# Kernel tuning notes

Measured on AMD Instinct MI355X. Metric: run time of the kernel, lower is better.

The kernel has to match this reference:

```python
import jax, jax.numpy as jnp
import numpy as np

EPS = 1e-5
DT_RANK = 64
N_STATE = 16


def _rmsnorm(x, w):
    var = jnp.mean(x * x, axis=-1, keepdims=True)
    return x * jax.lax.rsqrt(var + EPS) * w


def _softplus(x, beta=1.0, threshold=20.0):
    return jnp.where(beta * x > threshold, x, (1.0 / beta) * jnp.logaddexp(0.0, beta * x))


def _silu(x):
    return x * jax.nn.sigmoid(x)


def setup_inputs() -> dict:
    key = jax.random.key(0)
    ks = jax.random.split(key, 8)
    B, L, H = 2, 1024, 2048  # hidden_size = expand * d_model = 2048
    s = 0.02
    A = jnp.tile(jnp.arange(1.0, N_STATE + 1.0)[None, :], (H, 1))  # (H, 16)
    return {
        "x": jax.random.normal(ks[0], (B, L, H), jnp.float32),
        "norm_w": jnp.ones((H,), jnp.float32),
        "in_proj_w": jax.random.normal(ks[1], (2 * H, H), jnp.float32) * s,
        "conv_w": jax.random.normal(ks[2], (4, H, H), jnp.float32) * s,  # (K, Cin, Cout) LIO
        "conv_b": jnp.zeros((H,), jnp.float32),
        "x_proj_w": jax.random.normal(ks[3], (DT_RANK + 2 * N_STATE, H), jnp.float32) * s,
        "dt_proj_w": jax.random.normal(ks[4], (H, DT_RANK), jnp.float32) * s,
        "dt_proj_b": jnp.zeros((H,), jnp.float32),
        "A_log": jnp.log(A),
        "D": jnp.ones((H,), jnp.float32),
        "out_proj_w": jax.random.normal(ks[5], (H, H), jnp.float32) * s,
    }


def _scan_combine(left, right):
    aL, xL = left
    aR, xR = right
    return aR * aL, aR * xL + xR


def reference(x, norm_w, in_proj_w, conv_w, conv_b, x_proj_w, dt_proj_w, dt_proj_b, A_log, D, out_proj_w):
    B, L, H = x.shape
    h = _rmsnorm(x, norm_w)
    xz = h @ in_proj_w.T                      # (B, L, 2H)
    xc, z = jnp.split(xz, 2, axis=-1)         # each (B, L, H)
    # causal conv1d: mlx pads k-1 both sides then takes first L -> left pad only
    xc = jax.lax.conv_general_dilated(
        xc, conv_w, window_strides=(1,), padding=[(3, 0)],
        dimension_numbers=("NLC", "LIO", "NLC")) + conv_b
    xc = _silu(xc)
    # SSM
    A = -jnp.exp(A_log)                       # (H, N)
    dBC = xc @ x_proj_w.T                     # (B, L, dt_rank + 2N)
    delta = dBC[..., :DT_RANK]
    Bm = dBC[..., DT_RANK:DT_RANK + N_STATE]  # (B, L, N)
    Cm = dBC[..., DT_RANK + N_STATE:]         # (B, L, N)
    delta = _softplus(delta @ dt_proj_w.T + dt_proj_b)  # (B, L, H)
    deltaA = jnp.exp(delta[..., None] * A)              # (B, L, H, N)
    BX = (delta * xc)[..., None] * Bm[:, :, None, :]    # (B, L, H, N)
    _, hs = jax.lax.associative_scan(_scan_combine, (deltaA, BX), axis=1)
    y = jnp.einsum("blhn,bln->blh", hs, Cm) + D * xc
    out = (y * _silu(z)) @ out_proj_w.T
    return x + out
```

## Files before the change

kernel.cpp:

```cpp
#include <hip/hip_runtime.h>
#include <math.h>

typedef unsigned short u16;
typedef __bf16 bf16x8 __attribute__((ext_vector_type(8)));
typedef float f32x4 __attribute__((ext_vector_type(4)));
typedef unsigned short u16x8 __attribute__((ext_vector_type(8)));
typedef unsigned short u16x4 __attribute__((ext_vector_type(4)));

#define H 2048
#define LSEQ 1024
#define LP (LSEQ+3)
#define CL 32
#define NCH 32

__device__ __forceinline__ float bf2f(u16 u) {
    union { float f; unsigned int i; } x; x.i = ((unsigned int)u) << 16; return x.f;
}
__device__ __forceinline__ u16 f2bf(float f) {
    union { float f; unsigned int i; } x; x.f = f;
    unsigned int r = x.i + 0x7fffu + ((x.i >> 16) & 1u);
    return (u16)(r >> 16);
}

__device__ __forceinline__ void gload_lds16(const void* g, void* l) {
    __builtin_amdgcn_global_load_lds((const __attribute__((address_space(1))) void*)g,
                                     (__attribute__((address_space(3))) void*)l,
                                     16, 0, 0);
}

enum { EPI_XZ = 0, EPI_DELTA = 1, EPI_STORE = 5, EPI_P2 = 6 };

template<int EPI, bool APAD>
__launch_bounds__(512, 2)
__global__ void gemmA(const u16* __restrict__ A, const u16* __restrict__ B,
                      int lda, int ldb, long aZoff, long bZoff, int iters,
                      void* __restrict__ out0, void* __restrict__ out1,
                      void* __restrict__ out2, const float* __restrict__ aux) {
    __shared__ u16 As[5][128 * 32];
    __shared__ u16 Bs[5][256 * 32];
    const int flat = blockIdx.x + gridDim.x * (blockIdx.y + gridDim.y * blockIdx.z);
    const int xr = flat & 7;
    const int jj = flat >> 3;
    const int panel = xr + 8 * (jj >> 4);
    const int mI = jj & 15;
    const int m0 = mI * 128;
    const int yI = panel % gridDim.y;
    const int z  = panel / gridDim.y;
    const int n0 = yI * 256;
    const int tid = threadIdx.x;
    const int lane = tid & 63;
    const int w = tid >> 6;
    const int wr = w >> 2;
    const int wc = w & 3;

    long abase;
    if (APAD) {
        int b = m0 >> 10, l0 = m0 & 1023;
        abase = (long)(b * LP + l0) * lda;
    } else {
        abase = (long)m0 * lda;
    }
    const u16* Ag = A + abase + (long)z * aZoff;
    const u16* Bg = B + (long)n0 * ldb + (long)z * bZoff;

    const int sw8 = ((((lane & 15) >> 1) & 3) ^ (lane >> 4)) * 8;

    f32x4 acc[4][4];
#pragma unroll
    for (int i = 0; i < 4; i++)
#pragma unroll
        for (int j = 0; j < 4; j++) acc[i][j] = (f32x4){0.f, 0.f, 0.f, 0.f};

#define STG(s, bi)                                                                \
    {                                                                             \
        const int k0_ = (s) * 32;                                                 \
        {                                                                         \
            const int rA_ = tid >> 2;                                             \
            const int sgA_ = ((tid & 3) ^ ((rA_ >> 1) & 3)) * 8;                  \
            gload_lds16(Ag + (long)rA_ * lda + k0_ + sgA_, &As[bi][tid * 8]);     \
        }                                                                         \
        _Pragma("unroll")                                                         \
        for (int l_ = 0; l_ < 2; l_++) {                                          \
            const int idx_ = l_ * 512 + tid;                                      \
            const int rB_ = idx_ >> 2;                                            \
            const int sgB_ = ((idx_ & 3) ^ ((rB_ >> 1) & 3)) * 8;                 \
            gload_lds16(Bg + (long)rB_ * ldb + k0_ + sgB_, &Bs[bi][idx_ * 8]);    \
        }                                                                         \
    }

    STG(0, 0);
    if (iters > 1) STG(1, 1);
    if (iters > 2) STG(2, 2);
    if (iters > 3) STG(3, 3);
    {
        const int pre = iters < 4 ? iters : 4;
        if      (pre == 4) asm volatile("s_waitcnt vmcnt(9)" ::: "memory");
        else if (pre == 3) asm volatile("s_waitcnt vmcnt(6)" ::: "memory");
        else if (pre == 2) asm volatile("s_waitcnt vmcnt(3)" ::: "memory");
        else               asm volatile("s_waitcnt vmcnt(0)" ::: "memory");
    }
    __builtin_amdgcn_s_barrier();
    __builtin_amdgcn_sched_barrier(0);

    int cur = 0;
    for (int t = 0; t < iters; ++t) {
        const int sb = cur ? cur - 1 : 4;
        if (t + 4 < iters) STG(t + 4, sb);

        bf16x8 af[4], bfr[4];
#pragma unroll
        for (int i = 0; i < 4; i++) {
            const int row = wr * 64 + i * 16 + (lane & 15);
            af[i] = *(const bf16x8*)&As[cur][row * 32 + sw8];
        }
#pragma unroll
        for (int j = 0; j < 4; j++) {
            const int row = wc * 64 + j * 16 + (lane & 15);
            bfr[j] = *(const bf16x8*)&Bs[cur][row * 32 + sw8];
        }
        __builtin_amdgcn_s_setprio(1);
#pragma unroll
        for (int i = 0; i < 4; i++)
#pragma unroll
            for (int j = 0; j < 4; j++)
                acc[i][j] = __builtin_amdgcn_mfma_f32_16x16x32_bf16(af[i], bfr[j], acc[i][j], 0, 0, 0);
        __builtin_amdgcn_s_setprio(0);

        if (t < iters - 1) {
            const int lastst = (t + 4 < iters - 1) ? t + 4 : iters - 1;
            const int ahead = lastst - (t + 1);
            if      (ahead >= 3) asm volatile("s_waitcnt vmcnt(9)" ::: "memory");
            else if (ahead == 2) asm volatile("s_waitcnt vmcnt(6)" ::: "memory");
            else if (ahead == 1) asm volatile("s_waitcnt vmcnt(3)" ::: "memory");
            else                 asm volatile("s_waitcnt vmcnt(0)" ::: "memory");
            __builtin_amdgcn_s_barrier();
            __builtin_amdgcn_sched_barrier(0);
        }
        cur = (cur == 4) ? 0 : cur + 1;
    }
#undef STG

#pragma unroll
    for (int i = 0; i < 4; i++) {
#pragma unroll
        for (int j = 0; j < 4; j++) {
#pragma unroll
            for (int r = 0; r < 4; r++) {
                const int m = m0 + wr * 64 + i * 16 + ((lane >> 4) << 2) + r;
                const int n = n0 + wc * 64 + j * 16 + (lane & 15);
                float v = acc[i][j][r];
                if constexpr (EPI == EPI_XZ) {
                    const int b = m >> 10, l = m & 1023;
                    if (n < H) ((u16*)out0)[((long)(b * LP + l + 3)) * H + n] = f2bf(v);
                    else       ((u16*)out1)[(long)m * H + (n - H)] = f2bf(v);
                } else {
                    if (z == 0) {
                        ((float*)out0)[(long)m * H + n] = v;
                    } else {
                        float* p = (m < 1024) ? (float*)out1 : (float*)out2;
                        p[(long)(m & 1023) * H + n] = v;
                    }
                }
            }
        }
    }
}

template<int EPI, bool APAD>
__launch_bounds__(256)
__global__ void gemm_bt(const u16* __restrict__ A, const u16* __restrict__ B,
                        int K, long aZoff, long bZoff, int itersZ, int ldc,
                        void* __restrict__ out0, void* __restrict__ out1,
                        const float* __restrict__ bias) {
    __shared__ u16 As[128 * 32];
    __shared__ u16 Bs[128 * 32];
    const int m0 = blockIdx.x * 128;
    const int n0 = blockIdx.y * 128;
    const int z  = blockIdx.z;
    const int tid = threadIdx.x;
    const int lane = tid & 63;
    const int w = tid >> 6;
    const int wr = w >> 1, wc = w & 1;

    long abase = (long)m0 * K;
    const u16* Ag = A + abase + (long)z * aZoff;
    const u16* Bg = B + (long)n0 * K + (long)z * bZoff;

    const int sw8 = ((((lane & 15) >> 1) & 3) ^ (lane >> 4)) * 8;

    f32x4 acc[4][4];
#pragma unroll
    for (int i = 0; i < 4; i++)
#pragma unroll
        for (int j = 0; j < 4; j++) acc[i][j] = (f32x4){0.f, 0.f, 0.f, 0.f};

    for (int kt = 0; kt < itersZ; ++kt) {
        const int k0 = kt * 32;
        __syncthreads();
#pragma unroll
        for (int j = 0; j < 2; j++) {
            const int idx = j * 256 + tid;
            const int r = idx >> 2;
            const int segG = ((idx & 3) ^ ((r >> 1) & 3)) * 8;
            gload_lds16(Ag + (long)r * K + k0 + segG, &As[idx * 8]);
            gload_lds16(Bg + (long)r * K + k0 + segG, &Bs[idx * 8]);
        }
        __syncthreads();
        bf16x8 af[4], bfr[4];
#pragma unroll
        for (int i = 0; i < 4; i++) {
            const int row = wr * 64 + i * 16 + (lane & 15);
            af[i] = *(const bf16x8*)&As[row * 32 + sw8];
        }
#pragma unroll
        for (int j = 0; j < 4; j++) {
            const int row = wc * 64 + j * 16 + (lane & 15);
            bfr[j] = *(const bf16x8*)&Bs[row * 32 + sw8];
        }
#pragma unroll
        for (int i = 0; i < 4; i++)
#pragma unroll
            for (int j = 0; j < 4; j++)
                acc[i][j] = __builtin_amdgcn_mfma_f32_16x16x32_bf16(af[i], bfr[j], acc[i][j], 0, 0, 0);
    }

#pragma unroll
    for (int i = 0; i < 4; i++) {
#pragma unroll
        for (int j = 0; j < 4; j++) {
#pragma unroll
            for (int r = 0; r < 4; r++) {
                const int m = m0 + wr * 64 + i * 16 + ((lane >> 4) << 2) + r;
                const int n = n0 + wc * 64 + j * 16 + (lane & 15);
                float v = acc[i][j][r];
                if constexpr (EPI == EPI_DELTA) {
                    v += bias[n];
                    v = (v > 20.f) ? v : log1pf(expf(v));
                    ((float*)out0)[(long)m * H + n] = v;
                }
            }
        }
    }
}

template<int EPI, bool APAD>
__launch_bounds__(256)
__global__ void gemm128d(const u16* __restrict__ A, const u16* __restrict__ B,
                         int lda, int ldb, int iters,
                         long aZoff, long bZoff, long oZoff, int ldo,
                         void* __restrict__ out0, void* __restrict__ out1,
                         const float* __restrict__ aux) {
    __shared__ u16 As[6][128 * 32];
    __shared__ u16 Bs[6][128 * 32];
    const int m0 = blockIdx.y * 128;
    const int n0 = blockIdx.x * 128;
    const int z  = blockIdx.z;
    const int tid = threadIdx.x;
    const int lane = tid & 63;
    const int w = tid >> 6;
    const int wr = w >> 1, wc = w & 1;

    long abase = (long)m0 * lda;
    const u16* Ag = A + abase + (long)z * aZoff;
    const u16* Bg = B + (long)n0 * ldb + (long)z * bZoff;

    const int sw8 = ((((lane & 15) >> 1) & 3) ^ (lane >> 4)) * 8;

    f32x4 acc[4][4];
#pragma unroll
    for (int i = 0; i < 4; i++)
#pragma unroll
        for (int j = 0; j < 4; j++) acc[i][j] = (f32x4){0.f, 0.f, 0.f, 0.f};

#define STG(s, bi)                                                                \
    {                                                                             \
        const int k0_ = (s) * 32;                                                 \
        _Pragma("unroll")                                                         \
        for (int l_ = 0; l_ < 2; l_++) {                                          \
            const int idx_ = l_ * 256 + tid;                                      \
            const int r_ = idx_ >> 2;                                             \
            const int segG_ = ((idx_ & 3) ^ ((r_ >> 1) & 3)) * 8;                 \
            gload_lds16(Ag + (long)r_ * lda + k0_ + segG_, &As[bi][idx_ * 8]);    \
            gload_lds16(Bg + (long)r_ * ldb + k0_ + segG_, &Bs[bi][idx_ * 8]);    \
        }                                                                         \
    }

    STG(0, 0);
    if (iters > 1) STG(1, 1);
    if (iters > 2) STG(2, 2);
    if (iters > 3) STG(3, 3);
    if (iters > 4) STG(4, 4);
    {
        const int pre = iters < 5 ? iters : 5;
        if      (pre == 5) asm volatile("s_waitcnt vmcnt(16)" ::: "memory");
        else if (pre == 4) asm volatile("s_waitcnt vmcnt(12)" ::: "memory");
        else if (pre == 3) asm volatile("s_waitcnt vmcnt(8)" ::: "memory");
        else if (pre == 2) asm volatile("s_waitcnt vmcnt(4)" ::: "memory");
        else               asm volatile("s_waitcnt vmcnt(0)" ::: "memory");
    }
    __builtin_amdgcn_s_barrier();
    __builtin_amdgcn_sched_barrier(0);

    int cur = 0;
    for (int t = 0; t < iters; ++t) {
        const int sb = cur ? cur - 1 : 5;
        if (t + 5 < iters) STG(t + 5, sb);

        bf16x8 af[4], bfr[4];
#pragma unroll
        for (int i = 0; i < 4; i++) {
            const int row = wr * 64 + i * 16 + (lane & 15);
            af[i] = *(const bf16x8*)&As[cur][row * 32 + sw8];
        }
#pragma unroll
        for (int j = 0; j < 4; j++) {
            const int row = wc * 64 + j * 16 + (lane & 15);
            bfr[j] = *(const bf16x8*)&Bs[cur][row * 32 + sw8];
        }
        __builtin_amdgcn_s_setprio(1);
#pragma unroll
        for (int i = 0; i < 4; i++)
#pragma unroll
            for (int j = 0; j < 4; j++)
                acc[i][j] = __builtin_amdgcn_mfma_f32_16x16x32_bf16(af[i], bfr[j], acc[i][j], 0, 0, 0);
        __builtin_amdgcn_s_setprio(0);

        if (t < iters - 1) {
            const int lastst = (t + 5 < iters - 1) ? t + 5 : iters - 1;
            const int ahead = lastst - (t + 1);
            if      (ahead >= 4) asm volatile("s_waitcnt vmcnt(16)" ::: "memory");
            else if (ahead == 3) asm volatile("s_waitcnt vmcnt(12)" ::: "memory");
            else if (ahead == 2) asm volatile("s_waitcnt vmcnt(8)" ::: "memory");
            else if (ahead == 1) asm volatile("s_waitcnt vmcnt(4)" ::: "memory");
            else                 asm volatile("s_waitcnt vmcnt(0)" ::: "memory");
            __builtin_amdgcn_s_barrier();
            __builtin_amdgcn_sched_barrier(0);
        }
        cur = (cur == 5) ? 0 : cur + 1;
    }
#undef STG

#pragma unroll
    for (int i = 0; i < 4; i++) {
#pragma unroll
        for (int j = 0; j < 4; j++) {
#pragma unroll
            for (int r = 0; r < 4; r++) {
                const int m = m0 + wr * 64 + i * 16 + ((lane >> 4) << 2) + r;
                const int n = n0 + wc * 64 + j * 16 + (lane & 15);
                float v = acc[i][j][r];
                if constexpr (EPI == EPI_STORE) {
                    ((float*)out0 + (long)z * oZoff)[(long)m * ldo + n] = v;
                }
            }
        }
    }
}

__global__ void fin_conv2(const float* __restrict__ p0, const float* __restrict__ p1a,
                          const float* __restrict__ p1b, const float* __restrict__ bias,
                          u16* __restrict__ xcc) {
    const long i = ((long)blockIdx.x * 256 + threadIdx.x) * 4;
    f32x4 a = *(const f32x4*)(p0 + i);
    const long half = (long)1024 * 2048;
    const float* p1 = (i < half) ? p1a : p1b;
    const long i1 = (i < half) ? i : i - half;
    f32x4 b = *(const f32x4*)(p1 + i1);
    const int n = (int)(i & 2047);
    f32x4 bv = *(const f32x4*)(bias + n);
    u16x4 o;
#pragma unroll
    for (int j = 0; j < 4; j++) {
        float t = a[j] + b[j] + bv[j];
        o[j] = f2bf(t / (1.f + expf(-t)));
    }
    *(u16x4*)(xcc + i) = o;
}

__global__ void fin_out2(const float* __restrict__ p0, const float* __restrict__ p1a,
                         const float* __restrict__ p1b, const float* __restrict__ x,
                         float* __restrict__ out) {
    const long i = ((long)blockIdx.x * 256 + threadIdx.x) * 4;
    f32x4 a = *(const f32x4*)(p0 + i);
    const long half = (long)1024 * 2048;
    const float* p1 = (i < half) ? p1a : p1b;
    const long i1 = (i < half) ? i : i - half;
    f32x4 b = *(const f32x4*)(p1 + i1);
    f32x4 xv = *(const f32x4*)(x + i);
    f32x4 v;
#pragma unroll
    for (int j = 0; j < 4; j++) v[j] = xv[j] + a[j] + b[j];
    *(f32x4*)(out + i) = v;
}

__global__ void fin_dbc_k(const float* __restrict__ pacc, float* __restrict__ dbc,
                          u16* __restrict__ dbc64) {
    const int i = blockIdx.x * 256 + threadIdx.x;
    const int m = i >> 7, n = i & 127;
    float v = 0.f;
#pragma unroll
    for (int zz = 0; zz < 8; zz++) v += pacc[zz * 262144 + i];
    if (n < 96) dbc[m * 96 + n] = v;
    if (n < 64) dbc64[m * 64 + n] = f2bf(v);
}

__global__ void transpose_w(const float* __restrict__ in, u16* __restrict__ out) {
    __shared__ u16 s[64][72];
    const int tap = blockIdx.z;
    const long base = (long)tap * H * H;
    const int i0 = blockIdx.x * 64, o0 = blockIdx.y * 64;
    const int r = threadIdx.x >> 3;
    const int c = (threadIdx.x & 7) * 8;
#pragma unroll
    for (int rr = r; rr < 64; rr += 32) {
        f32x4 a = *(const f32x4*)&in[base + (long)(i0 + rr) * H + o0 + c];
        f32x4 b = *(const f32x4*)&in[base + (long)(i0 + rr) * H + o0 + c + 4];
#pragma unroll
        for (int j = 0; j < 4; j++) { s[rr][c + j] = f2bf(a[j]); s[rr][c + 4 + j] = f2bf(b[j]); }
    }
    __syncthreads();
#pragma unroll
    for (int rr = r; rr < 64; rr += 32) {
        u16x8 v;
#pragma unroll
        for (int j = 0; j < 8; j++) v[j] = s[c + j][rr];
        *(u16x8*)&out[(long)(o0 + rr) * (4 * H) + (long)tap * H + i0 + c] = v;
    }
}

__global__ void cast_f2b_k(const float* __restrict__ in, u16* __restrict__ out) {
    const long i = ((long)blockIdx.x * 256 + threadIdx.x) * 4;
    f32x4 v = *(const f32x4*)(in + i);
    u16x4 o;
#pragma unroll
    for (int j = 0; j < 4; j++) o[j] = f2bf(v[j]);
    *(u16x4*)(out + i) = o;
}

__global__ void pad_zero_k(u16* __restrict__ xcp) {
    const int i = blockIdx.x * 256 + threadIdx.x;
    const int b = i / (3 * H);
    const int r = i - b * 3 * H;
    xcp[(long)b * LP * H + r] = 0;
}

__global__ void xpw_k(const float* __restrict__ xp, u16* __restrict__ out) {
    const int i = blockIdx.x * 256 + threadIdx.x;
    const int r = i >> 11;
    out[i] = (r < 96) ? f2bf(xp[i]) : (u16)0;
}

__global__ void rmsnorm_k(const float* __restrict__ x, const float* __restrict__ w, u16* __restrict__ h) {
    const long base = (long)blockIdx.x * H;
    const int tid = threadIdx.x;
    f32x4 a = *(const f32x4*)&x[base + tid * 8];
    f32x4 b = *(const f32x4*)&x[base + tid * 8 + 4];
    float f[8];
    float ss = 0.f;
#pragma unroll
    for (int j = 0; j < 4; j++) { f[j] = a[j]; f[4 + j] = b[j]; }
#pragma unroll
    for (int j = 0; j < 8; j++) ss += f[j] * f[j];
#pragma unroll
    for (int m = 32; m > 0; m >>= 1) ss += __shfl_down(ss, m);
    __shared__ float red[4];
    if ((tid & 63) == 0) red[tid >> 6] = ss;
    __syncthreads();
    ss = red[0] + red[1] + red[2] + red[3];
    const float scale = rsqrtf(ss * (1.f / H) + 1e-5f);
    f32x4 wa = *(const f32x4*)&w[tid * 8];
    f32x4 wb = *(const f32x4*)&w[tid * 8 + 4];
    u16x8 o;
#pragma unroll
    for (int j = 0; j < 4; j++) { o[j] = f2bf(f[j] * scale * wa[j]); o[4 + j] = f2bf(f[4 + j] * scale * wb[j]); }
    *(u16x8*)&h[base + tid * 8] = o;
}

__launch_bounds__(256)
__global__ void scan_part1(const float* __restrict__ delta, const u16* __restrict__ xc,
                           const float* __restrict__ dbc, const float* __restrict__ alog,
                           u16* __restrict__ ssum, float* __restrict__ sdl_buf) {
    __shared__ float sB[CL * 16];
    const int tid = threadIdx.x;
    const int bc = blockIdx.x;
    const int b = bc >> 5, c = bc & 31;
    const int h = blockIdx.y * 256 + tid;
    const long tok0 = (long)b * LSEQ + c * CL;
    {
        const int r = tid >> 4, n = tid & 15;
        sB[tid] = dbc[(tok0 + r) * 96 + 64 + n];
        sB[tid + 256] = dbc[(tok0 + r + 16) * 96 + 64 + n];
    }
    __syncthreads();
    float An[16]; bool fast = true;
#pragma unroll
    for (int n = 0; n < 16; n++) {
        An[n] = -expf(alog[h * 16 + n]);
        fast = fast && (fabsf(An[n] + (float)(n + 1)) < 1e-3f * (n + 1));
    }
    float s[16];
#pragma unroll
    for (int n = 0; n < 16; n++) s[n] = 0.f;
    float sdl = 0.f;
    const float* dptr = delta + tok0 * H + h;
    const u16* xptr = xc + tok0 * H + h;
    float dl = dptr[0], xv = bf2f(xptr[0]);
    if (fast) {
        for (int j = 0; j < CL; j++) {
            const long jn = (j < CL - 1) ? (long)(j + 1) * H : (long)j * H;
            const float dl2 = dptr[jn]; const float xv2 = bf2f(xptr[jn]);
            sdl += dl;
            const float e1 = expf(-dl);
            const float u = dl * xv;
            const f32x4* Bv = (const f32x4*)&sB[j * 16];
            float ep = 1.f;
#pragma unroll
            for (int q = 0; q < 4; q++) {
                const f32x4 bb = Bv[q];
#pragma unroll
                for (int k = 0; k < 4; k++) { ep *= e1; s[q*4+k] = ep * s[q*4+k] + u * bb[k]; }
            }
            dl = dl2; xv = xv2;
        }
    } else {
        for (int j = 0; j < CL; j++) {
            const long jn = (j < CL - 1) ? (long)(j + 1) * H : (long)j * H;
            const float dl2 = dptr[jn]; const float xv2 = bf2f(xptr[jn]);
            sdl += dl;
            const float u = dl * xv;
            const f32x4* Bv = (const f32x4*)&sB[j * 16];
#pragma unroll
            for (int q = 0; q < 4; q++) {
                const f32x4 bb = Bv[q];
#pragma unroll
                for (int k = 0; k < 4; k++) { const float e = expf(dl * An[q*4+k]); s[q*4+k] = e * s[q*4+k] + u * bb[k]; }
            }
            dl = dl2; xv = xv2;
        }
    }
    u16x8 o0, o1;
#pragma unroll
    for (int n = 0; n < 8; n++) { o0[n] = f2bf(s[n]); o1[n] = f2bf(s[8 + n]); }
    const long sb = ((long)bc * H + h) * 16;
    *(u16x8*)&ssum[sb] = o0;
    *(u16x8*)&ssum[sb + 8] = o1;
    sdl_buf[(long)bc * H + h] = sdl;
}

__global__ void scan_mid(u16* __restrict__ ssum, const float* __restrict__ sdl_buf,
                         const float* __restrict__ alog) {
    const int tg = blockIdx.x * 256 + threadIdx.x;
    const int b = tg >> 15;
    const int rest = tg & 32767;
    const int h = rest >> 4, n = rest & 15;
    const float An = -expf(alog[h * 16 + n]);
    float S = 0.f;
    for (int c = 0; c < NCH; c++) {
        const long base = (long)(b * NCH + c) * H + h;
        const float a = expf(An * sdl_buf[base]);
        const long si = base * 16 + n;
        const float sloc = bf2f(ssum[si]);
        ssum[si] = f2bf(S);
        S = a * S + sloc;
    }
}

__launch_bounds__(256)
__global__ void scan_part3(const float* __restrict__ delta, const u16* __restrict__ xc,
                           const float* __restrict__ dbc, const float* __restrict__ alog,
                           const float* __restrict__ dvec, const u16* __restrict__ z,
                           const u16* __restrict__ ssum, u16* __restrict__ ybuf) {
    __shared__ float sB[CL * 16];
    __shared__ float sC[CL * 16];
    const int tid = threadIdx.x;
    const int bc = blockIdx.x;
    const int b = bc >> 5, c = bc & 31;
    const int h = blockIdx.y * 256 + tid;
    const long tok0 = (long)b * LSEQ + c * CL;
    {
        const int r = tid >> 4, n = tid & 15;
        sB[tid]       = dbc[(tok0 + r) * 96 + 64 + n];
        sB[tid + 256] = dbc[(tok0 + r + 16) * 96 + 64 + n];
        sC[tid]       = dbc[(tok0 + r) * 96 + 80 + n];
        sC[tid + 256] = dbc[(tok0 + r + 16) * 96 + 80 + n];
    }
    __syncthreads();
    float An[16]; bool fast = true;
#pragma unroll
    for (int n = 0; n < 16; n++) {
        An[n] = -expf(alog[h * 16 + n]);
        fast = fast && (fabsf(An[n] + (float)(n + 1)) < 1e-3f * (n + 1));
    }
    float s[16];
    {
        const long sb = ((long)bc * H + h) * 16;
        u16x8 i0 = *(const u16x8*)&ssum[sb];
        u16x8 i1 = *(const u16x8*)&ssum[sb + 8];
#pragma unroll
        for (int n = 0; n < 8; n++) { s[n] = bf2f(i0[n]); s[8 + n] = bf2f(i1[n]); }
    }
    const float Dh = dvec[h];
    const float* dptr = delta + tok0 * H + h;
    const u16* xptr = xc + tok0 * H + h;
    const u16* zptr = z + tok0 * H + h;
    u16* yptr = ybuf + tok0 * H + h;
    float dl = dptr[0], xv = bf2f(xptr[0]), zf = bf2f(zptr[0]);
    if (fast) {
        for (int j = 0; j < CL; j++) {
            const long jn = (j < CL - 1) ? (long)(j + 1) * H : (long)j * H;
            const float dl2 = dptr[jn]; const float xv2 = bf2f(xptr[jn]); const float zf2 = bf2f(zptr[jn]);
            const float e1 = expf(-dl);
            const float u = dl * xv;
            const f32x4* Bv = (const f32x4*)&sB[j * 16];
            const f32x4* Cv = (const f32x4*)&sC[j * 16];
            float ep = 1.f, y = 0.f;
#pragma unroll
            for (int q = 0; q < 4; q++) {
                const f32x4 bb = Bv[q], cc = Cv[q];
#pragma unroll
                for (int k = 0; k < 4; k++) {
                    ep *= e1;
                    s[q*4+k] = ep * s[q*4+k] + u * bb[k];
                    y += s[q*4+k] * cc[k];
                }
            }
            y += Dh * xv;
            const float g = zf / (1.f + expf(-zf));
            yptr[(long)j * H] = f2bf(y * g);
            dl = dl2; xv = xv2; zf = zf2;
        }
    } else {
        for (int j = 0; j < CL; j++) {
            const long jn = (j < CL - 1) ? (long)(j + 1) * H : (long)j * H;
            const float dl2 = dptr[jn]; const float xv2 = bf2f(xptr[jn]); const float zf2 = bf2f(zptr[jn]);
            const float u = dl * xv;
            const f32x4* Bv = (const f32x4*)&sB[j * 16];
            const f32x4* Cv = (const f32x4*)&sC[j * 16];
            float y = 0.f;
#pragma unroll
            for (int q = 0; q < 4; q++) {
                const f32x4 bb = Bv[q], cc = Cv[q];
#pragma unroll
                for (int k = 0; k < 4; k++) {
                    const float e = expf(dl * An[q*4+k]);
                    s[q*4+k] = e * s[q*4+k] + u * bb[k];
                    y += s[q*4+k] * cc[k];
                }
            }
            y += Dh * xv;
            const float g = zf / (1.f + expf(-zf));
            yptr[(long)j * H] = f2bf(y * g);
            dl = dl2; xv = xv2; zf = zf2;
        }
    }
}

extern "C" void kernel_launch(void* const* d_in, const int* in_sizes, int n_in,
                              void* d_out, int out_size, void* d_ws, size_t ws_size,
                              hipStream_t stream) {
    const float* x       = (const float*)d_in[0];
    const float* norm_w  = (const float*)d_in[1];
    const float* in_proj = (const float*)d_in[2];
    const float* conv_w  = (const float*)d_in[3];
    const float* conv_b  = (const float*)d_in[4];
    const float* x_proj  = (const float*)d_in[5];
    const float* dt_w    = (const float*)d_in[6];
    const float* dt_b    = (const float*)d_in[7];
    const float* a_log   = (const float*)d_in[8];
    const float* Dv      = (const float*)d_in[9];
    const float* out_w   = (const float*)d_in[10];
    float* out = (float*)d_out;

    char* ws = (char*)d_ws;
    u16*   xcp    = (u16*)(ws);
    u16*   hy     = (u16*)(ws + 8413184);
    float* hyF    = (float*)(ws + 8413184);
    u16*   z_buf  = (u16*)(ws + 16801792);
    u16*   wt     = (u16*)(ws + 25190400);
    float* dlt    = (float*)(ws + 25190400);
    u16*   y_buf  = (u16*)(ws + 41967616);
    u16*   ssum   = (u16*)(ws + 50356224);
    u16*   inw    = (u16*)(ws + 58744832);
    float* inwF   = (float*)(ws + 58744832);
    u16*   xpw    = (u16*)(ws + 75522048);
    float* dbc    = (float*)(ws + 76046336);
    u16*   dbc64  = (u16*)(ws + 76832768);
    u16*   dtw    = (u16*)(ws + 77094912);
    float* sdl    = (float*)(ws + 77225984);
    u16*   outw   = (u16*)(ws + 77750272);
    float* outwF  = (float*)(ws + 77750272);
    float* xcpF   = (float*)(ws);

    transpose_w<<<dim3(32, 32, 4), 256, 0, stream>>>(conv_w, wt);
    pad_zero_k<<<48, 256, 0, stream>>>(xcp);
    xpw_k<<<1024, 256, 0, stream>>>(x_proj, xpw);
    cast_f2b_k<<<8192, 256, 0, stream>>>(in_proj, inw);
    cast_f2b_k<<<128, 256, 0, stream>>>(dt_w, dtw);
    rmsnorm_k<<<2048, 256, 0, stream>>>(x, norm_w, hy);

    gemmA<EPI_XZ, false><<<dim3(16, 16, 1), 512, 0, stream>>>(
        hy, inw, 2048, 2048, 0, 0, 64, xcp, z_buf, nullptr, nullptr);

    gemmA<EPI_P2, true><<<dim3(16, 8, 2), 512, 0, stream>>>(
        xcp, wt, 2048, 4 * H, 4096, 4096, 128, inwF, hyF, outwF, nullptr);
    fin_conv2<<<4096, 256, 0, stream>>>(inwF, hyF, outwF, conv_b, (u16*)ws);

    cast_f2b_k<<<4096, 256, 0, stream>>>(out_w, outw);

    gemm128d<EPI_STORE, false><<<dim3(1, 16, 8), 256, 0, stream>>>(
        (u16*)ws, xpw, 2048, 2048, 8, 256, 256, 262144, 128, inwF, nullptr, nullptr);
    fin_dbc_k<<<1024, 256, 0, stream>>>(inwF, dbc, dbc64);

    gemm_bt<EPI_DELTA, false><<<dim3(16, 16, 1), 256, 0, stream>>>(
        dbc64, dtw, 64, 0, 0, 2, 0, dlt, nullptr, dt_b);

    scan_part1<<<dim3(64, 8), 256, 0, stream>>>(dlt, (u16*)ws, dbc, a_log, ssum, sdl);
    scan_mid<<<256, 256, 0, stream>>>(ssum, sdl, a_log);
    scan_part3<<<dim3(64, 8), 256, 0, stream>>>(dlt, (u16*)ws, dbc, a_log, Dv, z_buf, ssum, y_buf);

    gemmA<EPI_P2, false><<<dim3(16, 8, 2), 512, 0, stream>>>(
        y_buf, outw, 2048, 2048, 1024, 1024, 32, inwF, hyF, xcpF, nullptr);
    fin_out2<<<4096, 256, 0, stream>>>(inwF, hyF, xcpF, x, out);
}
```

Baseline: 502.3 us.

## Split GEMM k-step into phased LDS-read/MFMA groups with workgroup barriers

Restructures the inner GEMM loop so the LDS fragment reads and MFMAs are interleaved in three phases. Each phase has explicit s_barrier, lgkmcnt waits and sched_barriers, in a ping-pong style that lines up waves across the workgroup. The intent is to overlap LDS reads and global staging with MFMA issue and to get wave scheduling that favours the matrix pipe. In exchange it adds several workgroup barriers per k-iteration, which may stall waves and reduce latency hiding.

```diff
diff --git a/kernel.cpp b/kernel.cpp
--- a/kernel.cpp
+++ b/kernel.cpp
@@ -88,6 +88,10 @@
         }                                                                         \
     }
 
+#define LDA_F(i) (*(const bf16x8*)&As[cur][(wr * 64 + (i) * 16 + (lane & 15)) * 32 + sw8])
+#define LDB_F(j) (*(const bf16x8*)&Bs[cur][(wc * 64 + (j) * 16 + (lane & 15)) * 32 + sw8])
+#define MFMA(i, j, a, b) acc[i][j] = __builtin_amdgcn_mfma_f32_16x16x32_bf16((a), (b), acc[i][j], 0, 0, 0)
+
     STG(0, 0);
     if (iters > 1) STG(1, 1);
     if (iters > 2) STG(2, 2);
@@ -105,27 +109,45 @@
     int cur = 0;
     for (int t = 0; t < iters; ++t) {
         const int sb = cur ? cur - 1 : 4;
+        bf16x8 a0, a1, a2, a3, b0, b1, b2, b3;
+
+        a0 = LDA_F(0); a1 = LDA_F(1); b0 = LDB_F(0); b1 = LDB_F(1);
         if (t + 4 < iters) STG(t + 4, sb);
-
-        bf16x8 af[4], bfr[4];
-#pragma unroll
-        for (int i = 0; i < 4; i++) {
-            const int row = wr * 64 + i * 16 + (lane & 15);
-            af[i] = *(const bf16x8*)&As[cur][row * 32 + sw8];
-        }
-#pragma unroll
-        for (int j = 0; j < 4; j++) {
-            const int row = wc * 64 + j * 16 + (lane & 15);
-            bfr[j] = *(const bf16x8*)&Bs[cur][row * 32 + sw8];
-        }
+        __builtin_amdgcn_sched_barrier(0);
+        __builtin_amdgcn_s_barrier();
+        asm volatile("s_waitcnt lgkmcnt(0)" ::: "memory");
+        __builtin_amdgcn_sched_barrier(0);
         __builtin_amdgcn_s_setprio(1);
-#pragma unroll
-        for (int i = 0; i < 4; i++)
-#pragma unroll
-            for (int j = 0; j < 4; j++)
-                acc[i][j] = __builtin_amdgcn_mfma_f32_16x16x32_bf16(af[i], bfr[j], acc[i][j], 0, 0, 0);
+        MFMA(0, 0, a0, b0); MFMA(0, 1, a0, b1);
+        MFMA(1, 0, a1, b0); MFMA(1, 1, a1, b1);
         __builtin_amdgcn_s_setprio(0);
-
+        __builtin_amdgcn_sched_barrier(0);
+        __builtin_amdgcn_s_barrier();
+
+        b2 = LDB_F(2); b3 = LDB_F(3);
+        __builtin_amdgcn_sched_barrier(0);
+        __builtin_amdgcn_s_barrier();
+        asm volatile("s_waitcnt lgkmcnt(0)" ::: "memory");
+        __builtin_amdgcn_sched_barrier(0);
+        __builtin_amdgcn_s_setprio(1);
+        MFMA(0, 2, a0, b2); MFMA(0, 3, a0, b3);
+        MFMA(1, 2, a1, b2); MFMA(1, 3, a1, b3);
+        __builtin_amdgcn_s_setprio(0);
+        __builtin_amdgcn_sched_barrier(0);
+        __builtin_amdgcn_s_barrier();
+
+        a2 = LDA_F(2); a3 = LDA_F(3);
+        __builtin_amdgcn_sched_barrier(0);
+        __builtin_amdgcn_s_barrier();
+        asm volatile("s_waitcnt lgkmcnt(0)" ::: "memory");
+        __builtin_amdgcn_sched_barrier(0);
+        __builtin_amdgcn_s_setprio(1);
+        MFMA(2, 0, a2, b0); MFMA(2, 1, a2, b1);
+        MFMA(3, 0, a3, b0); MFMA(3, 1, a3, b1);
+        MFMA(2, 2, a2, b2); MFMA(2, 3, a2, b3);
+        MFMA(3, 2, a3, b2); MFMA(3, 3, a3, b3);
+        __builtin_amdgcn_s_setprio(0);
+        __builtin_amdgcn_sched_barrier(0);
         if (t < iters - 1) {
             const int lastst = (t + 4 < iters - 1) ? t + 4 : iters - 1;
             const int ahead = lastst - (t + 1);
@@ -139,6 +161,9 @@
         cur = (cur == 4) ? 0 : cur + 1;
     }
 #undef STG
+#undef LDA_F
+#undef LDB_F
+#undef MFMA
 
 #pragma unroll
     for (int i = 0; i < 4; i++) {
```

Measured after the change: 511.0 us. About the same (+1.7%).
